# Kernel tuning notes

Hardware: AMD Instinct MI355X
Metric: run time of the kernel (lower is better)

The kernel has to match this reference:

```python
import jax, jax.numpy as jnp
import numpy as np

EPSILON = 1.0


def setup_inputs() -> dict:
    key = jax.random.key(0)
    k1, k2 = jax.random.split(key)
    p = jax.random.normal(k1, (8192, 3), dtype=jnp.float32)       # dataset points [N, 3]
    u = jax.random.uniform(k2, (32768, 3), dtype=jnp.float32)     # uniform noise  [M, 3]
    return {"p": p, "u": u}


def reference(p, u):
    # UniformDataset: box bounds from dataset extent (grads flow through min/max)
    mm = jnp.min(p, axis=0)  # [3]
    mx = jnp.max(p, axis=0)  # [3]
    # UniformSample: M uniform samples in the bounding box (vectorized, no per-sample loop)
    s = u * (mx - mm) + mm   # [M, 3]
    # dist_from_to: min euclidean distance from each sample to the dataset.
    # Expansion ||s||^2 + ||p||^2 - 2 s.p avoids the [M, N, 3] difference tensor.
    d2 = (jnp.sum(s * s, axis=1)[:, None]
          + jnp.sum(p * p, axis=1)[None, :]
          - 2.0 * (s @ p.T))                      # [M, N]
    dist = jnp.sqrt(jnp.clip(jnp.min(d2, axis=1), 0.0))  # [M]
    # Threshold filter. Torch does boolean indexing (data-dependent shape);
    # for jit-compatibility we keep fixed shape [M] and zero out rejected rows.
    mask = dist > EPSILON                         # [M]
    aug = jnp.where(mask[:, None], s, jnp.zeros_like(s))  # [M, 3]
    # concat_original=True: [p; accepted uniform samples (padded)]
    return jnp.concatenate([p, aug], axis=0)      # [N + M, 3]
```

## Files before the change

kernel.cpp:

```cpp
#include <hip/hip_runtime.h>
#include <hip/hip_bf16.h>
#include <float.h>


typedef __attribute__((ext_vector_type(8))) short short8;
typedef __attribute__((ext_vector_type(16))) float float16;

constexpr float MARGIN = 1e-2f;
constexpr int WV = 8;
constexpr int SPBLK = 64;

__device__ __forceinline__ unsigned short f2bf(float f) {
  unsigned u = __float_as_uint(f);
  unsigned r = (u + 0x7FFFu + ((u >> 16) & 1u)) >> 16;
  return (unsigned short)r;
}
__device__ __forceinline__ float bf2f(unsigned short b) {
  return __uint_as_float(((unsigned)b) << 16);
}

__global__ __launch_bounds__(256) void prep_kernel(
    const float* __restrict__ p, int N,
    float* __restrict__ out, float4* __restrict__ P4, float* __restrict__ mmx,
    short8* __restrict__ Ap) {
  const int tid = threadIdx.x;
  if (blockIdx.x == 0) {
    float mn0 = FLT_MAX, mn1 = FLT_MAX, mn2 = FLT_MAX;
    float mx0 = -FLT_MAX, mx1 = -FLT_MAX, mx2 = -FLT_MAX;
    for (int j = tid; j < N; j += 256) {
      float x = p[3 * j], y = p[3 * j + 1], z = p[3 * j + 2];
      mn0 = fminf(mn0, x); mx0 = fmaxf(mx0, x);
      mn1 = fminf(mn1, y); mx1 = fmaxf(mx1, y);
      mn2 = fminf(mn2, z); mx2 = fmaxf(mx2, z);
    }
    for (int off = 32; off; off >>= 1) {
      mn0 = fminf(mn0, __shfl_xor(mn0, off));
      mn1 = fminf(mn1, __shfl_xor(mn1, off));
      mn2 = fminf(mn2, __shfl_xor(mn2, off));
      mx0 = fmaxf(mx0, __shfl_xor(mx0, off));
      mx1 = fmaxf(mx1, __shfl_xor(mx1, off));
      mx2 = fmaxf(mx2, __shfl_xor(mx2, off));
    }
    __shared__ float smn[4][3], smx[4][3];
    const int w = tid >> 6;
    if ((tid & 63) == 0) {
      smn[w][0] = mn0; smn[w][1] = mn1; smn[w][2] = mn2;
      smx[w][0] = mx0; smx[w][1] = mx1; smx[w][2] = mx2;
    }
    __syncthreads();
    if (tid == 0) {
      for (int k = 0; k < 3; ++k) {
        float a = smn[0][k], b = smx[0][k];
        for (int w2 = 1; w2 < 4; ++w2) {
          a = fminf(a, smn[w2][k]);
          b = fmaxf(b, smx[w2][k]);
        }
        mmx[k] = a;
        mmx[3 + k] = b;
      }
    }
  } else {
    const int j = (blockIdx.x - 1) * 256 + tid;
    if (j < N) {
      float x = p[3 * j], y = p[3 * j + 1], z = p[3 * j + 2];
      out[3 * j] = x; out[3 * j + 1] = y; out[3 * j + 2] = z;
      float n2 = __fadd_rn(__fadd_rn(__fmul_rn(x, x), __fmul_rn(y, y)),
                           __fmul_rn(z, z));
      P4[j] = make_float4(x, y, z, n2);

      unsigned short hx = f2bf(x), hy = f2bf(y), hz = f2bf(z);
      unsigned short lx = f2bf(x - bf2f(hx));
      unsigned short ly = f2bf(y - bf2f(hy));
      unsigned short lz = f2bf(z - bf2f(hz));
      unsigned short p2h = f2bf(n2);
      unsigned short p2l = f2bf(n2 - bf2f(p2h));
      const unsigned short one = 0x3F80;

      const int tile = j >> 5, r = j & 31;
      short8 h0, h1;
      h0[0] = (short)hx; h0[1] = (short)hy; h0[2] = (short)hz;
      h0[3] = (short)lx; h0[4] = (short)ly; h0[5] = (short)lz;
      h0[6] = (short)hx; h0[7] = (short)hy;
      h1[0] = (short)hz; h1[1] = (short)one; h1[2] = (short)one;
      h1[3] = (short)p2h; h1[4] = (short)p2l;
      h1[5] = 0; h1[6] = 0; h1[7] = 0;
      Ap[tile * 64 + r] = h0;
      Ap[tile * 64 + 32 + r] = h1;
    }
  }
}

__device__ __forceinline__ float min16(float16 c) {
  float a0 = fminf(fminf(c[0], c[1]), c[2]);
  float a1 = fminf(fminf(c[3], c[4]), c[5]);
  float a2 = fminf(fminf(c[6], c[7]), c[8]);
  float a3 = fminf(fminf(c[9], c[10]), c[11]);
  float a4 = fminf(fminf(c[12], c[13]), c[14]);
  return fminf(fminf(fminf(a0, a1), fminf(a2, a3)), fminf(a4, c[15]));
}

__global__ __launch_bounds__(64 * WV) void dist_kernel(
    const float* __restrict__ u, int M, int N,
    const float4* __restrict__ P4, const float* __restrict__ mmx,
    const short8* __restrict__ Ap, float* __restrict__ out) {
  const int tid = threadIdx.x;
  const int lane = tid & 63;
  const int wv = tid >> 6;
  const int sbase = blockIdx.x * SPBLK;

  const float mm0 = mmx[0], mm1 = mmx[1], mm2 = mmx[2];
  const float r0v = __fsub_rn(mmx[3], mm0);
  const float r1v = __fsub_rn(mmx[4], mm1);
  const float r2v = __fsub_rn(mmx[5], mm2);

  short8 B[2];
  const bool hi = lane >= 32;
#pragma unroll
  for (int f = 0; f < 2; ++f) {
    int sc = min(sbase + f * 32 + (lane & 31), M - 1);
    float sx = __fadd_rn(__fmul_rn(u[3 * sc], r0v), mm0);
    float sy = __fadd_rn(__fmul_rn(u[3 * sc + 1], r1v), mm1);
    float sz = __fadd_rn(__fmul_rn(u[3 * sc + 2], r2v), mm2);
    float s2 = __fadd_rn(
        __fadd_rn(__fmul_rn(sx, sx), __fmul_rn(sy, sy)), __fmul_rn(sz, sz));
    unsigned short shx = f2bf(sx), shy = f2bf(sy), shz = f2bf(sz);
    unsigned short slx = f2bf(sx - bf2f(shx));
    unsigned short sly = f2bf(sy - bf2f(shy));
    unsigned short slz = f2bf(sz - bf2f(shz));
    unsigned short n2shx = f2bf(-2.0f * bf2f(shx));
    unsigned short n2shy = f2bf(-2.0f * bf2f(shy));
    unsigned short n2shz = f2bf(-2.0f * bf2f(shz));
    unsigned short n2slx = f2bf(-2.0f * bf2f(slx));
    unsigned short n2sly = f2bf(-2.0f * bf2f(sly));
    unsigned short n2slz = f2bf(-2.0f * bf2f(slz));
    unsigned short s2h = f2bf(s2);
    unsigned short s2l = f2bf(s2 - bf2f(s2h));
    const unsigned short one = 0x3F80;
    short8 b;
    b[0] = (short)(hi ? n2slz : n2shx);
    b[1] = (short)(hi ? s2h : n2shy);
    b[2] = (short)(hi ? s2l : n2shz);
    b[3] = (short)(hi ? one : n2shx);
    b[4] = (short)(hi ? one : n2shy);
    b[5] = (short)(hi ? 0 : n2shz);
    b[6] = (short)(hi ? 0 : n2slx);
    b[7] = (short)(hi ? 0 : n2sly);
    B[f] = b;
  }

  const int NT = N >> 5;
  const int TPW = NT / WV;
  const int tbase = wv * TPW;
  const short8* __restrict__ ap = Ap + tbase * 64 + lane;
  const float16 cz = (float16)0.0f;

  float run0 = FLT_MAX, run1 = FLT_MAX;
  short8 aC = ap[0];
  short8 aN = ap[64];
  for (int it = 0; it < TPW; ++it) {
    short8 aF = ap[(it + 2 < TPW ? it + 2 : it) * 64];
    float16 c0 = __builtin_amdgcn_mfma_f32_32x32x16_bf16(aC, B[0], cz, 0, 0, 0);
    float16 c1 = __builtin_amdgcn_mfma_f32_32x32x16_bf16(aC, B[1], cz, 0, 0, 0);
    run0 = fminf(run0, min16(c0));
    run1 = fminf(run1, min16(c1));
    aC = aN; aN = aF;
  }
  run0 = fminf(run0, __shfl_xor(run0, 32));
  run1 = fminf(run1, __shfl_xor(run1, 32));

  __shared__ float part[WV][SPBLK];
  if (lane < 32) part[wv][lane] = run0;
  else           part[wv][32 + (lane & 31)] = run1;

  __shared__ float s_sx[SPBLK], s_sy[SPBLK], s_sz[SPBLK], s_s2[SPBLK];
  __shared__ int s_keep[SPBLK];
  __shared__ int s_bl[SPBLK];
  __shared__ int s_nbl;
  __shared__ float s_red[WV];
  if (tid == 0) s_nbl = 0;
  __syncthreads();

  if (tid < SPBLK && sbase + tid < M) {
    int sc = sbase + tid;
    float sx = __fadd_rn(__fmul_rn(u[3 * sc], r0v), mm0);
    float sy = __fadd_rn(__fmul_rn(u[3 * sc + 1], r1v), mm1);
    float sz = __fadd_rn(__fmul_rn(u[3 * sc + 2], r2v), mm2);
    float s2 = __fadd_rn(
        __fadd_rn(__fmul_rn(sx, sx), __fmul_rn(sy, sy)), __fmul_rn(sz, sz));
    s_sx[tid] = sx; s_sy[tid] = sy; s_sz[tid] = sz; s_s2[tid] = s2;
    float q = part[0][tid];
#pragma unroll
    for (int w = 1; w < WV; ++w) q = fminf(q, part[w][tid]);
    s_keep[tid] = q > 1.0f;
    if (fabsf(q - 1.0f) <= MARGIN) {
      int idx = atomicAdd(&s_nbl, 1);
      s_bl[idx] = tid;
    }
  }
  __syncthreads();

  const int nbl = s_nbl;
  for (int i = 0; i < nbl; ++i) {
    const int t = s_bl[i];
    const float m2x = -2.0f * s_sx[t];
    const float m2y = -2.0f * s_sy[t];
    const float m2z = -2.0f * s_sz[t];
    float dm = FLT_MAX;
    for (int j = tid; j < N; j += 64 * WV) {
      float4 qq = P4[j];
      float tt = fmaf(m2x, qq.x, fmaf(m2y, qq.y, fmaf(m2z, qq.z, qq.w)));
      dm = fminf(dm, tt);
    }
    dm = fminf(dm, __shfl_xor(dm, 1));
    dm = fminf(dm, __shfl_xor(dm, 2));
    dm = fminf(dm, __shfl_xor(dm, 4));
    dm = fminf(dm, __shfl_xor(dm, 8));
    dm = fminf(dm, __shfl_xor(dm, 16));
    dm = fminf(dm, __shfl_xor(dm, 32));
    if (lane == 0) s_red[wv] = dm;
    __syncthreads();
    if (tid == 0) {
      float d = s_red[0];
#pragma unroll
      for (int w = 1; w < WV; ++w) d = fminf(d, s_red[w]);
      float d2 = __fadd_rn(s_s2[t], d);
      float dist = sqrtf(fmaxf(d2, 0.0f));
      s_keep[t] = dist > 1.0f;
    }
    __syncthreads();
  }

  if (tid < SPBLK && sbase + tid < M) {
    const bool keep = s_keep[tid] != 0;
    float* o = out + (size_t)(N + sbase + tid) * 3;
    o[0] = keep ? s_sx[tid] : 0.0f;
    o[1] = keep ? s_sy[tid] : 0.0f;
    o[2] = keep ? s_sz[tid] : 0.0f;
  }
}

extern "C" void kernel_launch(void* const* d_in, const int* in_sizes, int n_in,
                              void* d_out, int out_size, void* d_ws, size_t ws_size,
                              hipStream_t stream) {
  const float* p = (const float*)d_in[0];
  const float* u = (const float*)d_in[1];
  const int N = in_sizes[0] / 3;
  const int M = in_sizes[1] / 3;
  float* out = (float*)d_out;

  float* mmx = (float*)d_ws;
  float4* P4 = (float4*)((char*)d_ws + 256);
  short8* Ap = (short8*)((char*)d_ws + 262144);

  const int pblocks = (N + 255) / 256;
  prep_kernel<<<dim3(1 + pblocks), 256, 0, stream>>>(p, N, out, P4, mmx, Ap);

  const int sblocks = (M + SPBLK - 1) / SPBLK;
  dist_kernel<<<dim3(sblocks), dim3(64 * WV), 0, stream>>>(u, M, N, P4, mmx,
                                                           Ap, out);
}
```

Before: 32.18 us.

## Widen block to 128 samples and 16 waves, keep elementwise running minima

Each block now handles 128 samples (four B fragments) with 16 waves, so every loaded A tile feeds four MFMAs instead of two. Per-tile horizontal min16 reductions are replaced by elementwise running minima kept in accumulator-sized registers, with a single reduction after the loop. The goal is to cut A-fragment load traffic and reduction ALU work per MFMA. In exchange it uses far more VGPRs (four float16 running minima), launches half as many blocks, and gives each wave fewer tiles to iterate.

```diff
diff --git a/kernel.cpp b/kernel.cpp
--- a/kernel.cpp
+++ b/kernel.cpp
@@ -7,8 +7,9 @@
 typedef __attribute__((ext_vector_type(16))) float float16;
 
 constexpr float MARGIN = 1e-2f;
-constexpr int WV = 8;
-constexpr int SPBLK = 64;
+constexpr int WV = 16;
+constexpr int SPBLK = 128;
+constexpr int NFRAG = SPBLK / 32;
 
 __device__ __forceinline__ unsigned short f2bf(float f) {
   unsigned u = __float_as_uint(f);
@@ -113,10 +114,10 @@
   const float r1v = __fsub_rn(mmx[4], mm1);
   const float r2v = __fsub_rn(mmx[5], mm2);
 
-  short8 B[2];
+  short8 B[NFRAG];
   const bool hi = lane >= 32;
 #pragma unroll
-  for (int f = 0; f < 2; ++f) {
+  for (int f = 0; f < NFRAG; ++f) {
     int sc = min(sbase + f * 32 + (lane & 31), M - 1);
     float sx = __fadd_rn(__fmul_rn(u[3 * sc], r0v), mm0);
     float sy = __fadd_rn(__fmul_rn(u[3 * sc + 1], r1v), mm1);
@@ -150,27 +151,33 @@
 
   const int NT = N >> 5;
   const int TPW = NT / WV;
-  const int tbase = wv * TPW;
-  const short8* __restrict__ ap = Ap + tbase * 64 + lane;
+  const short8* __restrict__ ap = Ap + (wv * TPW) * 64 + lane;
   const float16 cz = (float16)0.0f;
 
-  float run0 = FLT_MAX, run1 = FLT_MAX;
+  float16 rc[NFRAG];
+#pragma unroll
+  for (int f = 0; f < NFRAG; ++f) rc[f] = (float16)FLT_MAX;
+
   short8 aC = ap[0];
   short8 aN = ap[64];
   for (int it = 0; it < TPW; ++it) {
     short8 aF = ap[(it + 2 < TPW ? it + 2 : it) * 64];
-    float16 c0 = __builtin_amdgcn_mfma_f32_32x32x16_bf16(aC, B[0], cz, 0, 0, 0);
-    float16 c1 = __builtin_amdgcn_mfma_f32_32x32x16_bf16(aC, B[1], cz, 0, 0, 0);
-    run0 = fminf(run0, min16(c0));
-    run1 = fminf(run1, min16(c1));
+#pragma unroll
+    for (int f = 0; f < NFRAG; ++f) {
+      float16 c = __builtin_amdgcn_mfma_f32_32x32x16_bf16(aC, B[f], cz, 0, 0, 0);
+#pragma unroll
+      for (int r = 0; r < 16; ++r) rc[f][r] = fminf(rc[f][r], c[r]);
+    }
     aC = aN; aN = aF;
   }
-  run0 = fminf(run0, __shfl_xor(run0, 32));
-  run1 = fminf(run1, __shfl_xor(run1, 32));
 
   __shared__ float part[WV][SPBLK];
-  if (lane < 32) part[wv][lane] = run0;
-  else           part[wv][32 + (lane & 31)] = run1;
+#pragma unroll
+  for (int f = 0; f < NFRAG; ++f) {
+    float v = min16(rc[f]);
+    v = fminf(v, __shfl_xor(v, 32));
+    part[wv][f * 32 + (lane & 31)] = v;
+  }
 
   __shared__ float s_sx[SPBLK], s_sy[SPBLK], s_sz[SPBLK], s_s2[SPBLK];
   __shared__ int s_keep[SPBLK];
```

Result: slower. 47.76 us (+48.4%).
